# Kernel tuning notes

Hardware: AMD Instinct MI355X
Metric: run time of the kernel (lower is better)

## Reference

```python
import jax, jax.numpy as jnp
import numpy as np

G = 16          # horizontal stripes
K = 4           # latents per stripe
TEMP = 0.125
TOPK_RATIO = 0.125
GATE_THR = 0.05
EPS = 1e-6
KSZ = 3


def setup_inputs() -> dict:
    key = jax.random.key(0)
    k1, k2 = jax.random.split(key)
    x = jax.random.normal(k1, (64, 256, 64, 44), dtype=jnp.float32)
    latent_basis = jax.random.normal(k2, (G, K, 256), dtype=jnp.float32)
    return {"x": x, "latent_basis": latent_basis}


def _avg_pool3(x):
    # x: [n, g, c, sh, w]; 3x3 avg pool, stride 1, pad 1, count_include_pad=True
    s = jax.lax.reduce_window(x, 0.0, jax.lax.add,
                              (1, 1, 1, KSZ, KSZ), (1, 1, 1, 1, 1),
                              [(0, 0), (0, 0), (0, 0), (1, 1), (1, 1)])
    return s / float(KSZ * KSZ)


def _l2norm(v, axis=-1):
    return v / jnp.maximum(jnp.linalg.norm(v, axis=axis, keepdims=True), 1e-12)


def reference(x, latent_basis):
    n, c, h, w = x.shape
    sh = h // G
    p = sh * w
    # split into horizontal stripes: [n, g, c, sh, w]
    xr = x.reshape(n, c, G, sh, w).transpose(0, 2, 1, 3, 4)
    support_feat = _avg_pool3(xr)
    feat_flat = xr.transpose(0, 1, 3, 4, 2).reshape(n, G, p, c)          # ngpc
    support_flat = support_feat.transpose(0, 1, 3, 4, 2).reshape(n, G, p, c)

    # active mask from detached feature energy
    e = jax.lax.stop_gradient(xr).astype(jnp.float32)
    fe = jnp.mean(e * e, axis=2)                                          # n g sh w
    fe = fe / jnp.maximum(jnp.max(fe, axis=(-2, -1), keepdims=True), EPS)
    active = (fe > GATE_THR).astype(jnp.float32)
    fallback = (fe > 0).astype(jnp.float32)
    use_fb = jnp.sum(active, axis=(-2, -1), keepdims=True) <= 0
    active = jnp.where(use_fb, fallback, active).reshape(n, G, p)

    # cosine-similarity routing
    sfn = _l2norm(support_flat)
    lbn = _l2norm(latent_basis)                                           # g k c
    logits = jnp.einsum('ngpc,gkc->ngpk', sfn, lbn) / TEMP
    route_prob = jax.nn.softmax(logits, axis=-1)
    support = route_prob * active[..., None]                              # n g p k
    pool_w = support / jnp.maximum(jnp.sum(support, axis=2, keepdims=True), EPS)
    tokens = jnp.einsum('ngpk,ngpc->ngkc', pool_w, feat_flat)
    tokens = tokens.transpose(0, 3, 1, 2).reshape(n, c, G * K)            # n c (g k)

    # top-k presence
    kk = max(1, min(p, int(p * TOPK_RATIO)))
    topv, _ = jax.lax.top_k(support.transpose(0, 1, 3, 2), kk)            # n g k kk
    presence = jnp.mean(topv, axis=-1).reshape(n, G * K)
    presence = presence / jnp.maximum(jnp.sum(presence, axis=1, keepdims=True), EPS)

    # scatter per-stripe maps back into full-resolution zero tensors
    eye = jnp.eye(G, dtype=support.dtype)
    loc_s = support.reshape(n, G, sh, w, K).transpose(0, 1, 4, 2, 3)      # n g k sh w
    loc_p = pool_w.reshape(n, G, sh, w, K).transpose(0, 1, 4, 2, 3)
    smap = jnp.einsum('ngksw,gG->ngkGsw', loc_s, eye).reshape(n, G * K, h, w)
    pmap = jnp.einsum('ngksw,gG->ngkGsw', loc_p, eye).reshape(n, G * K, h, w)
    support_flat_global = smap.transpose(0, 2, 3, 1).reshape(n, h * w, G * K)
    pool_weights_flat_global = pmap.transpose(0, 2, 3, 1).reshape(n, h * w, G * K)

    return (tokens.astype(x.dtype), presence.astype(x.dtype),
            support_flat_global.astype(x.dtype), pool_weights_flat_global.astype(x.dtype))
```

## Files before the change

kernel.cpp:

```cpp
#include <hip/hip_runtime.h>
#include <math.h>

#define GG   16
#define KK   4
#define NN   64
#define CC   256
#define SHH  4
#define WW   44
#define PP   176
#define HWSZ 2816
#define CHW  720896
#define TOPKK 22

template<int CTRL, int RMASK>
__device__ __forceinline__ float dpp0(float v) {
    return __int_as_float(__builtin_amdgcn_update_dpp(
        0, __float_as_int(v), CTRL, RMASK, 0xF, true));
}
__device__ __forceinline__ float nbrL(float v) { return dpp0<0x138, 0xF>(v); }
__device__ __forceinline__ float nbrR(float v) { return dpp0<0x130, 0xF>(v); }

__device__ __forceinline__ float wave_sum63(float v) {
    v += dpp0<0x111, 0xF>(v);
    v += dpp0<0x112, 0xF>(v);
    v += dpp0<0x114, 0xF>(v);
    v += dpp0<0x118, 0xF>(v);
    v += dpp0<0x142, 0xA>(v);
    v += dpp0<0x143, 0xC>(v);
    return v;
}
__device__ __forceinline__ float bcast63(float v) {
    return __int_as_float(__builtin_amdgcn_readlane(__float_as_int(v), 63));
}
__device__ __forceinline__ float wave_sum_all(float v) { return bcast63(wave_sum63(v)); }

__device__ __forceinline__ float wave_max_nn(float v) {
    v = fmaxf(v, dpp0<0x111, 0xF>(v));
    v = fmaxf(v, dpp0<0x112, 0xF>(v));
    v = fmaxf(v, dpp0<0x114, 0xF>(v));
    v = fmaxf(v, dpp0<0x118, 0xF>(v));
    v = fmaxf(v, dpp0<0x142, 0xA>(v));
    v = fmaxf(v, dpp0<0x143, 0xC>(v));
    return bcast63(v);
}

__global__ __launch_bounds__(512, 8) void routing_kernel(
    const float* __restrict__ x, const float* __restrict__ lb_raw,
    float* __restrict__ pw_ws, float* __restrict__ pres_ws,
    float4* __restrict__ outS, float4* __restrict__ outP) {
    const int g = blockIdx.x;
    const int n = blockIdx.y;
    const int tid = threadIdx.x;
    const int w = __builtin_amdgcn_readfirstlane(tid >> 6);
    const int lane = tid & 63;
    const bool al = lane < WW;

    __shared__ float4 pd[8][PP];
    __shared__ float2 pnf[8][PP];
    __shared__ float4 lbn_lds[CC];
    __shared__ float redA[4], redB[4], zred[4][4];
    float4* sup4 = pd[2];
    float4* pw4  = pd[4];

    if (w < 4) {
        const float* row = lb_raw + ((size_t)g * KK + w) * CC;
        float v0 = row[lane], v1 = row[lane + 64], v2 = row[lane + 128], v3 = row[lane + 192];
        float ss = v0 * v0 + v1 * v1 + v2 * v2 + v3 * v3;
        float tot = wave_sum_all(ss);
        float sc = (1.0f / 9.0f) / fmaxf(sqrtf(tot), 1e-12f);
        float* dst = (float*)lbn_lds;
        dst[lane * 4 + w]         = v0 * sc;
        dst[(lane + 64) * 4 + w]  = v1 * sc;
        dst[(lane + 128) * 4 + w] = v2 * sc;
        dst[(lane + 192) * 4 + w] = v3 * sc;
    }
    __syncthreads();

    const float* xb = x + (size_t)n * CHW + g * PP;
    const int c0 = w * 32;

    float4 dk[4];
    float nr[4] = {0, 0, 0, 0}, fe[4] = {0, 0, 0, 0};
    #pragma unroll
    for (int s = 0; s < 4; ++s) dk[s] = make_float4(0, 0, 0, 0);

    const float* xp = xb + (size_t)c0 * HWSZ + lane;
    float c0r = 0, c1r = 0, c2r = 0, c3r = 0;
    float n0r = 0, n1r = 0, n2r = 0, n3r = 0;
    if (al) {
        c0r = xp[0]; c1r = xp[44]; c2r = xp[88]; c3r = xp[132];
        n0r = xp[HWSZ]; n1r = xp[HWSZ + 44]; n2r = xp[HWSZ + 88]; n3r = xp[HWSZ + 132];
    }
    xp += 2 * HWSZ;
    #pragma unroll 1
    for (int i = 0; i < 32; ++i) {
        float f0 = 0, f1 = 0, f2 = 0, f3 = 0;
        if (i < 30 && al) { f0 = xp[0]; f1 = xp[44]; f2 = xp[88]; f3 = xp[132]; }
        xp += HWSZ;
        float4 lbv = lbn_lds[c0 + i];
        fe[0] += c0r * c0r; fe[1] += c1r * c1r; fe[2] += c2r * c2r; fe[3] += c3r * c3r;
        float h0 = c0r + nbrL(c0r) + nbrR(c0r);
        float h1 = c1r + nbrL(c1r) + nbrR(c1r);
        float h2 = c2r + nbrL(c2r) + nbrR(c2r);
        float h3 = c3r + nbrL(c3r) + nbrR(c3r);
        float p0 = h0 + h1;
        float p1 = p0 + h2;
        float t23 = h2 + h3;
        float p2 = h1 + t23;
        float p3 = t23;
        nr[0] += p0 * p0; nr[1] += p1 * p1; nr[2] += p2 * p2; nr[3] += p3 * p3;
        dk[0].x += p0 * lbv.x; dk[0].y += p0 * lbv.y; dk[0].z += p0 * lbv.z; dk[0].w += p0 * lbv.w;
        dk[1].x += p1 * lbv.x; dk[1].y += p1 * lbv.y; dk[1].z += p1 * lbv.z; dk[1].w += p1 * lbv.w;
        dk[2].x += p2 * lbv.x; dk[2].y += p2 * lbv.y; dk[2].z += p2 * lbv.z; dk[2].w += p2 * lbv.w;
        dk[3].x += p3 * lbv.x; dk[3].y += p3 * lbv.y; dk[3].z += p3 * lbv.z; dk[3].w += p3 * lbv.w;
        c0r = n0r; c1r = n1r; c2r = n2r; c3r = n3r;
        n0r = f0; n1r = f1; n2r = f2; n3r = f3;
    }
    if (al) {
        #pragma unroll
        for (int s = 0; s < 4; ++s) {
            pd[w][s * 44 + lane]  = dk[s];
            pnf[w][s * 44 + lane] = make_float2(nr[s], fe[s]);
        }
    }
    __syncthreads();

    if (tid < PP) {
        float4 a = pd[0][tid];
        #pragma unroll
        for (int ww = 1; ww < 8; ++ww) {
            float4 b = pd[ww][tid];
            a.x += b.x; a.y += b.y; a.z += b.z; a.w += b.w;
        }
        pd[0][tid] = a;
    } else if (tid >= 256 && tid < 256 + PP) {
        const int p = tid - 256;
        float2 a = pnf[0][p];
        #pragma unroll
        for (int ww = 1; ww < 8; ++ww) {
            float2 b = pnf[ww][p];
            a.x += b.x; a.y += b.y;
        }
        pnf[0][p] = a;
    }
    __syncthreads();

    const int s4 = w & 3;
    const int pix = s4 * 44 + (al ? lane : 0);
    float4 dv = pd[0][pix];
    float2 nf = pnf[0][pix];
    float nrm = nf.x;
    float fev = nf.y * (1.0f / 256.0f);

    float fmw = wave_max_nn(al ? fev : 0.0f);
    if (w < 4 && lane == 0) redA[s4] = fmw;
    __syncthreads();
    float femax = fmaxf(fmaxf(redA[0], redA[1]), fmaxf(redA[2], redA[3]));
    float den = fmaxf(femax, 1e-6f);
    bool pa = al && ((fev / den) > 0.05f);
    unsigned long long bl = __ballot((int)pa);
    if (w < 4 && lane == 0) redB[s4] = (float)__popcll(bl);
    __syncthreads();
    float cnt = redB[0] + redB[1] + redB[2] + redB[3];
    float actv = pa ? 1.0f : 0.0f;
    if (cnt <= 0.0f) actv = (al && (fev > 0.0f)) ? 1.0f : 0.0f;

    float inv = 72.0f / fmaxf(sqrtf(nrm), 9e-12f);
    float L0 = dv.x * inv, L1 = dv.y * inv, L2 = dv.z * inv, L3 = dv.w * inv;
    float mx = fmaxf(fmaxf(L0, L1), fmaxf(L2, L3));
    float e0 = expf(L0 - mx), e1 = expf(L1 - mx), e2 = expf(L2 - mx), e3 = expf(L3 - mx);
    float esum = e0 + e1 + e2 + e3;
    float sc = actv / esum;
    float s0 = e0 * sc, s1 = e1 * sc, s2 = e2 * sc, s3 = e3 * sc;

    float z0 = wave_sum63(s0), z1 = wave_sum63(s1), z2 = wave_sum63(s2), z3 = wave_sum63(s3);
    if (w < 4 && lane == 63) { zred[s4][0] = z0; zred[s4][1] = z1; zred[s4][2] = z2; zred[s4][3] = z3; }
    __syncthreads();
    float Z0 = zred[0][0] + zred[1][0] + zred[2][0] + zred[3][0];
    float Z1 = zred[0][1] + zred[1][1] + zred[2][1] + zred[3][1];
    float Z2 = zred[0][2] + zred[1][2] + zred[2][2] + zred[3][2];
    float Z3 = zred[0][3] + zred[1][3] + zred[2][3] + zred[3][3];
    float q0 = s0 / fmaxf(Z0, 1e-6f);
    float q1 = s1 / fmaxf(Z1, 1e-6f);
    float q2 = s2 / fmaxf(Z2, 1e-6f);
    float q3 = s3 / fmaxf(Z3, 1e-6f);

    if (w < 4 && al) {
        float4 sv = make_float4(s0, s1, s2, s3);
        float4 qv = make_float4(q0, q1, q2, q3);
        sup4[pix] = sv;
        pw4[pix]  = qv;
        ((float4*)pw_ws)[(size_t)(n * GG + g) * PP + pix] = qv;
    }
    __syncthreads();

    if (w < 4) {
        const float* supf = (const float*)sup4;
        const int k = w;
        float v0 = supf[lane * 4 + k];
        float v1 = supf[(lane + 64) * 4 + k];
        float v2 = (lane < PP - 128) ? supf[(lane + 128) * 4 + k] : -1e30f;
        float tks = 0.0f;
        for (int it = 0; it < TOPKK; ++it) {
            float lm = fmaxf(v0, fmaxf(v1, v2));
            float M = wave_max_nn(lm);
            tks += M;
            unsigned long long mk = __ballot((int)(lm == M));
            int src = __ffsll(mk) - 1;
            if (lane == src) {
                if (v0 == M)      v0 = -1e30f;
                else if (v1 == M) v1 = -1e30f;
                else              v2 = -1e30f;
            }
        }
        if (lane == 0) pres_ws[(size_t)n * 64 + g * KK + k] = tks * (1.0f / (float)TOPKK);
    }

    {
        const size_t obase = ((size_t)n * HWSZ + (size_t)g * PP) * 16;
        const float4 z = make_float4(0, 0, 0, 0);
        #pragma unroll 1
        for (int j = tid; j < PP * 16; j += 512) {
            const int px = j >> 4, q = j & 15;
            const bool hit = (q == g);
            outS[obase + j] = hit ? sup4[px] : z;
            outP[obase + j] = hit ? pw4[px]  : z;
        }
    }
}

__global__ __launch_bounds__(256, 8) void token_kernel(
    const float* __restrict__ x, const float* __restrict__ pw_ws,
    float* __restrict__ tok_out) {
    const int g = blockIdx.x & 15;
    const int chunk = blockIdx.x >> 4;
    const int n = blockIdx.y;
    const int w = __builtin_amdgcn_readfirstlane(threadIdx.x >> 6);
    const int lane = threadIdx.x & 63;

    const float4* pwq = (const float4*)pw_ws + (size_t)(n * GG + g) * PP;
    float4 pwa = pwq[lane];
    float4 pwb = pwq[lane + 64];
    float4 pwc = (lane < 48) ? pwq[lane + 128] : make_float4(0, 0, 0, 0);

    const int cb = chunk * 64 + w * 16;
    const float* xp = x + (size_t)n * CHW + g * PP + (size_t)cb * HWSZ + lane;
    float* tokg = tok_out + (size_t)n * CC * 64 + g * KK + (size_t)cb * 64;

    float a0 = xp[0];
    float a1 = xp[64];
    float a2 = (lane < 48) ? xp[128] : 0.0f;
    xp += HWSZ;
    #pragma unroll 1
    for (int i = 0; i < 16; ++i) {
        float b0 = 0, b1 = 0, b2 = 0;
        if (i < 15) {
            b0 = xp[0]; b1 = xp[64];
            if (lane < 48) b2 = xp[128];
        }
        xp += HWSZ;
        float t0 = a0 * pwa.x + a1 * pwb.x + a2 * pwc.x;
        float t1 = a0 * pwa.y + a1 * pwb.y + a2 * pwc.y;
        float t2 = a0 * pwa.z + a1 * pwb.z + a2 * pwc.z;
        float t3 = a0 * pwa.w + a1 * pwb.w + a2 * pwc.w;
        t0 = wave_sum63(t0); t1 = wave_sum63(t1); t2 = wave_sum63(t2); t3 = wave_sum63(t3);
        if (lane == 63) {
            *(float4*)(tokg + (size_t)i * 64) = make_float4(t0, t1, t2, t3);
        }
        a0 = b0; a1 = b1; a2 = b2;
    }
}

__global__ __launch_bounds__(64) void presence_kernel(
    const float* __restrict__ pres_ws, float* __restrict__ outp) {
    const int n = blockIdx.x;
    const int lane = threadIdx.x;
    float v = pres_ws[(size_t)n * 64 + lane];
    float tot = wave_sum_all(v);
    outp[(size_t)n * 64 + lane] = v / fmaxf(tot, 1e-6f);
}

extern "C" void kernel_launch(void* const* d_in, const int* in_sizes, int n_in,
                              void* d_out, int out_size, void* d_ws, size_t ws_size,
                              hipStream_t stream) {
    const float* x = (const float*)d_in[0];
    const float* lb = (const float*)d_in[1];
    float* ws = (float*)d_ws;
    float* pres_ws = ws;
    float* pw_ws   = pres_ws + 4096;

    float* out = (float*)d_out;
    float* tok  = out;
    float* pres = out + 1048576;
    float* outS = out + 1052672;
    float* outP = outS + 11534336;

    routing_kernel<<<dim3(GG, NN), 512, 0, stream>>>(
        x, lb, pw_ws, pres_ws, (float4*)outS, (float4*)outP);
    token_kernel<<<dim3(GG * 4, NN), 256, 0, stream>>>(x, pw_ws, tok);
    presence_kernel<<<NN, 64, 0, stream>>>(pres_ws, pres);
}
```

Before: 342.2 us.

## Fuse token pooling into routing kernel using LDS-resident pool weights

The separate token kernel is removed and the weighted channel pooling now runs at the end of the routing kernel. Pool weights are read straight from shared memory instead of a global workspace, and each of the 8 waves covers 32 channels. This drops one kernel launch and the pool-weight round trip through global memory. It may also let x be reused from cache after the routing pass. The cost is longer per-block work with less parallelism (1024 blocks instead of 4096 for this stage) and a tail that is serialized after the zero-fill stores.

```diff
diff --git a/kernel.cpp b/kernel.cpp
--- a/kernel.cpp
+++ b/kernel.cpp
@@ -46,8 +46,9 @@
 
 __global__ __launch_bounds__(512, 8) void routing_kernel(
     const float* __restrict__ x, const float* __restrict__ lb_raw,
-    float* __restrict__ pw_ws, float* __restrict__ pres_ws,
-    float4* __restrict__ outS, float4* __restrict__ outP) {
+    float* __restrict__ pres_ws,
+    float4* __restrict__ outS, float4* __restrict__ outP,
+    float* __restrict__ tok_out) {
     const int g = blockIdx.x;
     const int n = blockIdx.y;
     const int tid = threadIdx.x;
@@ -186,11 +187,8 @@
     float q3 = s3 / fmaxf(Z3, 1e-6f);
 
     if (w < 4 && al) {
-        float4 sv = make_float4(s0, s1, s2, s3);
-        float4 qv = make_float4(q0, q1, q2, q3);
-        sup4[pix] = sv;
-        pw4[pix]  = qv;
-        ((float4*)pw_ws)[(size_t)(n * GG + g) * PP + pix] = qv;
+        sup4[pix] = make_float4(s0, s1, s2, s3);
+        pw4[pix]  = make_float4(q0, q1, q2, q3);
     }
     __syncthreads();
 
@@ -227,47 +225,36 @@
             outP[obase + j] = hit ? pw4[px]  : z;
         }
     }
-}
-
-__global__ __launch_bounds__(256, 8) void token_kernel(
-    const float* __restrict__ x, const float* __restrict__ pw_ws,
-    float* __restrict__ tok_out) {
-    const int g = blockIdx.x & 15;
-    const int chunk = blockIdx.x >> 4;
-    const int n = blockIdx.y;
-    const int w = __builtin_amdgcn_readfirstlane(threadIdx.x >> 6);
-    const int lane = threadIdx.x & 63;
-
-    const float4* pwq = (const float4*)pw_ws + (size_t)(n * GG + g) * PP;
-    float4 pwa = pwq[lane];
-    float4 pwb = pwq[lane + 64];
-    float4 pwc = (lane < 48) ? pwq[lane + 128] : make_float4(0, 0, 0, 0);
-
-    const int cb = chunk * 64 + w * 16;
-    const float* xp = x + (size_t)n * CHW + g * PP + (size_t)cb * HWSZ + lane;
-    float* tokg = tok_out + (size_t)n * CC * 64 + g * KK + (size_t)cb * 64;
-
-    float a0 = xp[0];
-    float a1 = xp[64];
-    float a2 = (lane < 48) ? xp[128] : 0.0f;
-    xp += HWSZ;
-    #pragma unroll 1
-    for (int i = 0; i < 16; ++i) {
-        float b0 = 0, b1 = 0, b2 = 0;
-        if (i < 15) {
-            b0 = xp[0]; b1 = xp[64];
-            if (lane < 48) b2 = xp[128];
-        }
-        xp += HWSZ;
-        float t0 = a0 * pwa.x + a1 * pwb.x + a2 * pwc.x;
-        float t1 = a0 * pwa.y + a1 * pwb.y + a2 * pwc.y;
-        float t2 = a0 * pwa.z + a1 * pwb.z + a2 * pwc.z;
-        float t3 = a0 * pwa.w + a1 * pwb.w + a2 * pwc.w;
-        t0 = wave_sum63(t0); t1 = wave_sum63(t1); t2 = wave_sum63(t2); t3 = wave_sum63(t3);
-        if (lane == 63) {
-            *(float4*)(tokg + (size_t)i * 64) = make_float4(t0, t1, t2, t3);
-        }
-        a0 = b0; a1 = b1; a2 = b2;
+
+    {
+        float4 pwa = pw4[lane];
+        float4 pwb = pw4[lane + 64];
+        float4 pwc = (lane < 48) ? pw4[lane + 128] : make_float4(0, 0, 0, 0);
+        const float* xq = xb + (size_t)c0 * HWSZ + lane;
+        float* tokg = tok_out + ((size_t)n * CC + c0) * 64 + g * KK;
+
+        float a0 = xq[0];
+        float a1 = xq[64];
+        float a2 = (lane < 48) ? xq[128] : 0.0f;
+        xq += HWSZ;
+        #pragma unroll 1
+        for (int i = 0; i < 32; ++i) {
+            float b0 = 0, b1 = 0, b2 = 0;
+            if (i < 31) {
+                b0 = xq[0]; b1 = xq[64];
+                if (lane < 48) b2 = xq[128];
+            }
+            xq += HWSZ;
+            float t0 = a0 * pwa.x + a1 * pwb.x + a2 * pwc.x;
+            float t1 = a0 * pwa.y + a1 * pwb.y + a2 * pwc.y;
+            float t2 = a0 * pwa.z + a1 * pwb.z + a2 * pwc.z;
+            float t3 = a0 * pwa.w + a1 * pwb.w + a2 * pwc.w;
+            t0 = wave_sum63(t0); t1 = wave_sum63(t1); t2 = wave_sum63(t2); t3 = wave_sum63(t3);
+            if (lane == 63) {
+                *(float4*)(tokg + (size_t)i * 64) = make_float4(t0, t1, t2, t3);
+            }
+            a0 = b0; a1 = b1; a2 = b2;
+        }
     }
 }
 
@@ -287,7 +274,6 @@
     const float* lb = (const float*)d_in[1];
     float* ws = (float*)d_ws;
     float* pres_ws = ws;
-    float* pw_ws   = pres_ws + 4096;
 
     float* out = (float*)d_out;
     float* tok  = out;
@@ -296,7 +282,6 @@
     float* outP = outS + 11534336;
 
     routing_kernel<<<dim3(GG, NN), 512, 0, stream>>>(
-        x, lb, pw_ws, pres_ws, (float4*)outS, (float4*)outP);
-    token_kernel<<<dim3(GG * 4, NN), 256, 0, stream>>>(x, pw_ws, tok);
+        x, lb, pres_ws, (float4*)outS, (float4*)outP, tok);
     presence_kernel<<<NN, 64, 0, stream>>>(pres_ws, pres);
 }
```

Measured after the change: 337.2 us. No clear change (-1.5%).
